# Kernel optimization log

Hardware: AMD Instinct MI355X
Metric: run time of the kernel (lower is better)

The kernel has to match this reference:

```python
import jax, jax.numpy as jnp
import numpy as np

SIGMAS = [1.0, 2.0, 4.0, 8.0, 16.0]
EPS = 0.05
ITERS = 30
N, M, D = 8192, 8192, 128


def _sqdist(X, Y):
    # ||x_i - y_j||^2, [n, m]
    d2 = (jnp.sum(X * X, axis=1)[:, None]
          + jnp.sum(Y * Y, axis=1)[None, :]
          - 2.0 * (X @ Y.T))
    return jnp.maximum(d2, 0.0)


def _ms_rbf(X, Y):
    d2 = _sqdist(X, Y)
    K = jnp.zeros_like(d2)
    for s in SIGMAS:  # small fixed loop over scales
        K = K + jnp.exp(-d2 / (2.0 * s * s))
    return K / float(len(SIGMAS))


def _sinkhorn_uniform(cost, eps, iters):
    n, m = cost.shape
    dtype = cost.dtype
    log_a = jnp.asarray(-np.log(float(n)), dtype)
    log_b = jnp.asarray(-np.log(float(m)), dtype)
    log_K = -(cost - jax.lax.stop_gradient(jnp.min(cost))) / eps

    def step(carry, _):
        log_u, log_v = carry
        log_u = log_a - jax.scipy.special.logsumexp(log_K + log_v[None, :], axis=1)
        log_v = log_b - jax.scipy.special.logsumexp(log_K + log_u[:, None], axis=0)
        return (log_u, log_v), None

    init = (jnp.zeros((n,), dtype), jnp.zeros((m,), dtype))
    (log_u, log_v), _ = jax.lax.scan(step, init, None, length=iters)
    return jnp.exp(log_u[:, None] + log_K + log_v[None, :])


def setup_inputs() -> dict:
    key = jax.random.key(0)
    kx, ky = jax.random.split(key)
    X = jax.random.normal(kx, (N, D), dtype=jnp.float32)
    Y = jax.random.normal(ky, (M, D), dtype=jnp.float32)
    return {"X": X, "Y": Y}


def reference(X, Y):
    Kxx = jnp.mean(_ms_rbf(X, X))
    Kyy = jnp.mean(_ms_rbf(Y, Y))
    Kxy = _ms_rbf(X, Y)
    cost = 1.0 / float(X.shape[0] * Y.shape[0]) - Kxy
    Gamma = _sinkhorn_uniform(cost, EPS, ITERS)
    Kxy_weighted = jnp.sum(Gamma * Kxy)
    return Kxx + Kyy - 2.0 * Kxy_weighted
```

## Files before the change

### kernel.cpp

```cpp
#include <hip/hip_runtime.h>
#include <math.h>

#define NR 8192
#define DDIM 128

static constexpr float LOG_AB2 = -13.0f;
static constexpr float OFF2    = -28.853900817779268f;
static constexpr float C8      = 0.11315255222658537f;
static constexpr float DQK8    = 1.0f / 255.0f;
static constexpr float E1 = -0.7213475204444817f;
static constexpr float E2 = -0.18033688011112043f;
static constexpr float E3 = -0.045084220027780107f;
static constexpr float E4 = -0.011271055006945027f;
static constexpr float E5 = -0.0028177637517362567f;

typedef __attribute__((ext_vector_type(8))) short  s16x8;
typedef __attribute__((ext_vector_type(4))) float  f32x4;

#if defined(__has_builtin)
#if __has_builtin(__builtin_amdgcn_exp2f)
#define EX2_IMPL(x) __builtin_amdgcn_exp2f(x)
#endif
#endif
#ifndef EX2_IMPL
extern "C" __device__ float __ocml_native_exp2_f32(float);
#define EX2_IMPL(x) __ocml_native_exp2_f32(x)
#endif
__device__ inline float ex2(float x) { return EX2_IMPL(x); }

__device__ inline unsigned short bf16rn(float f) {
    const unsigned u = __float_as_uint(f);
    return (unsigned short)((u + 0x7FFFu + ((u >> 16) & 1u)) >> 16);
}

__global__ __launch_bounds__(256) void conv_k(const float* __restrict__ X,
                                              unsigned short* __restrict__ hi,
                                              unsigned short* __restrict__ lo) {
    const int i = blockIdx.x * 1024 + threadIdx.x * 4;
    const float4 v = *reinterpret_cast<const float4*>(&X[i]);
    const float f[4] = {v.x, v.y, v.z, v.w};
    ushort4 h, l;
    unsigned short hh[4], ll[4];
#pragma unroll
    for (int j = 0; j < 4; ++j) {
        const unsigned short a = bf16rn(f[j]);
        const float hf = __uint_as_float((unsigned)a << 16);
        hh[j] = a;
        ll[j] = bf16rn(f[j] - hf);
    }
    h.x = hh[0]; h.y = hh[1]; h.z = hh[2]; h.w = hh[3];
    l.x = ll[0]; l.y = ll[1]; l.z = ll[2]; l.w = ll[3];
    *reinterpret_cast<ushort4*>(&hi[i]) = h;
    *reinterpret_cast<ushort4*>(&lo[i]) = l;
}

__global__ __launch_bounds__(256) void rownorm_k(const float* __restrict__ X,
                                                 float* __restrict__ nrm) {
    const int lane = threadIdx.x & 63;
    const int w    = threadIdx.x >> 6;
    const int row  = blockIdx.x * 4 + w;
    const float2 v = *reinterpret_cast<const float2*>(&X[(size_t)row * DDIM + lane * 2]);
    float s = v.x * v.x + v.y * v.y;
#pragma unroll
    for (int off = 32; off; off >>= 1) s += __shfl_xor(s, off);
    if (lane == 0) nrm[row] = s;
}

template <int MODE>
__global__ __launch_bounds__(256) void gemm_mfma_k(const unsigned short* __restrict__ XH,
                                                   const unsigned short* __restrict__ XL,
                                                   const unsigned short* __restrict__ YH,
                                                   const unsigned short* __restrict__ YL,
                                                   const float* __restrict__ nxp,
                                                   const float* __restrict__ nyp,
                                                   unsigned char* __restrict__ K8,
                                                   double* __restrict__ sums) {
    int bm, bn;
    const unsigned short *AH, *AL, *BH, *BL;
    const float *na, *nb;
    if (MODE == 0) {
        bm = blockIdx.x; bn = blockIdx.y;
        AH = XH; AL = XL; BH = YH; BL = YL; na = nxp; nb = nyp;
    } else {
        const int lin = blockIdx.x;
        int i = (int)((129.0f - sqrtf(16641.0f - 8.0f * (float)lin)) * 0.5f);
        while (i * 64 - i * (i - 1) / 2 > lin) --i;
        while ((i + 1) * 64 - (i + 1) * i / 2 <= lin) ++i;
        bm = i;
        bn = i + (lin - (i * 64 - i * (i - 1) / 2));
        const int sel = blockIdx.y;
        AH = BH = sel ? YH : XH;
        AL = BL = sel ? YL : XL;
        na = nb = sel ? nyp : nxp;
    }
    __shared__ unsigned short AsH[128 * 40], AsL[128 * 40], BsH[128 * 40], BsL[128 * 40];

    const int t    = threadIdx.x;
    const int lane = t & 63;
    const int w    = t >> 6;
    const int wr   = w >> 1, wc = w & 1;
    const int l15  = lane & 15, lg = lane >> 4;

    f32x4 acc[4][4];
#pragma unroll
    for (int mi = 0; mi < 4; ++mi)
#pragma unroll
        for (int ni = 0; ni < 4; ++ni) acc[mi][ni] = (f32x4){0.f, 0.f, 0.f, 0.f};

    const unsigned short* gAH = AH + (size_t)(bm * 128) * DDIM;
    const unsigned short* gAL = AL + (size_t)(bm * 128) * DDIM;
    const unsigned short* gBH = BH + (size_t)(bn * 128) * DDIM;
    const unsigned short* gBL = BL + (size_t)(bn * 128) * DDIM;

    for (int kc = 0; kc < 4; ++kc) {
        const int k0 = kc * 32;
        __syncthreads();
#pragma unroll
        for (int q = 0; q < 2; ++q) {
            const int idx = t + q * 256;
            const int row = idx >> 2, seg = idx & 3;
            const int go = row * DDIM + k0 + seg * 8;
            const int so = row * 40 + seg * 8;
            *reinterpret_cast<uint4*>(&AsH[so]) = *reinterpret_cast<const uint4*>(&gAH[go]);
            *reinterpret_cast<uint4*>(&AsL[so]) = *reinterpret_cast<const uint4*>(&gAL[go]);
            *reinterpret_cast<uint4*>(&BsH[so]) = *reinterpret_cast<const uint4*>(&gBH[go]);
            *reinterpret_cast<uint4*>(&BsL[so]) = *reinterpret_cast<const uint4*>(&gBL[go]);
        }
        __syncthreads();

        s16x8 bh[4], bl[4];
#pragma unroll
        for (int ni = 0; ni < 4; ++ni) {
            const int off = (wc * 64 + ni * 16 + l15) * 40 + lg * 8;
            bh[ni] = *reinterpret_cast<const s16x8*>(&BsH[off]);
            bl[ni] = *reinterpret_cast<const s16x8*>(&BsL[off]);
        }
#pragma unroll
        for (int mi = 0; mi < 4; ++mi) {
            const int off = (wr * 64 + mi * 16 + l15) * 40 + lg * 8;
            const s16x8 ah = *reinterpret_cast<const s16x8*>(&AsH[off]);
            const s16x8 al = *reinterpret_cast<const s16x8*>(&AsL[off]);
#pragma unroll
            for (int ni = 0; ni < 4; ++ni) {
                acc[mi][ni] = __builtin_amdgcn_mfma_f32_16x16x32_bf16(ah, bh[ni], acc[mi][ni], 0, 0, 0);
                acc[mi][ni] = __builtin_amdgcn_mfma_f32_16x16x32_bf16(ah, bl[ni], acc[mi][ni], 0, 0, 0);
                acc[mi][ni] = __builtin_amdgcn_mfma_f32_16x16x32_bf16(al, bh[ni], acc[mi][ni], 0, 0, 0);
            }
        }
    }

    const int mBase = bm * 128 + wr * 64;
    const int nBase = bn * 128 + wc * 64;
    float nbv[4];
#pragma unroll
    for (int ni = 0; ni < 4; ++ni) nbv[ni] = nb[nBase + ni * 16 + l15];

    if (MODE == 0) {
#pragma unroll
        for (int mi = 0; mi < 4; ++mi) {
#pragma unroll
            for (int j = 0; j < 4; ++j) {
                const int m = mBase + mi * 16 + lg * 4 + j;
                const float nav = na[m];
                unsigned char* krow = &K8[(size_t)m * NR + nBase + l15];
#pragma unroll
                for (int ni = 0; ni < 4; ++ni) {
                    float d2 = fmaf(-2.f, acc[mi][ni][j], nav + nbv[ni]);
                    d2 = fmaxf(d2, 0.f);
                    const float kv = 0.2f * (ex2(d2 * E1) + ex2(d2 * E2) + ex2(d2 * E3) +
                                             ex2(d2 * E4) + ex2(d2 * E5));
                    krow[ni * 16] = (unsigned char)__float2uint_rn(kv * 255.f);
                }
            }
        }
    } else {
        double lsum = 0.0;
#pragma unroll
        for (int mi = 0; mi < 4; ++mi) {
#pragma unroll
            for (int j = 0; j < 4; ++j) {
                const int m = mBase + mi * 16 + lg * 4 + j;
                const float nav = na[m];
                float rs = 0.f;
#pragma unroll
                for (int ni = 0; ni < 4; ++ni) {
                    float d2 = fmaf(-2.f, acc[mi][ni][j], nav + nbv[ni]);
                    d2 = fmaxf(d2, 0.f);
                    rs += 0.2f * (ex2(d2 * E1) + ex2(d2 * E2) + ex2(d2 * E3) +
                                  ex2(d2 * E4) + ex2(d2 * E5));
                }
                lsum += (double)rs;
            }
        }
        if (bn > bm) lsum *= 2.0;
#pragma unroll
        for (int o = 32; o; o >>= 1) lsum += __shfl_xor(lsum, o);
        if (lane == 0) atomicAdd(&sums[1 + blockIdx.y], lsum);
    }
}

__global__ __launch_bounds__(256) void init_lv_k(float* __restrict__ log_v) {
    log_v[blockIdx.x * 256 + threadIdx.x] = OFF2;
}

__global__ __launch_bounds__(256) void sink_row_k(const unsigned char* __restrict__ K8,
                                                  const float* __restrict__ log_v,
                                                  float* __restrict__ log_u) {
    __shared__ float red[4][8];
    const int t  = threadIdx.x;
    const int r0 = blockIdx.x * 8;
    const float4* Lv4 = reinterpret_cast<const float4*>(log_v);
    float s[8];
#pragma unroll
    for (int r = 0; r < 8; ++r) s[r] = 0.f;
#pragma unroll
    for (int p = 0; p < 2; ++p) {
        const int g = t + p * 256;
        const float4 l0 = Lv4[4 * g + 0];
        const float4 l1 = Lv4[4 * g + 1];
        const float4 l2 = Lv4[4 * g + 2];
        const float4 l3 = Lv4[4 * g + 3];
        const float lvv[16] = {l0.x, l0.y, l0.z, l0.w, l1.x, l1.y, l1.z, l1.w,
                               l2.x, l2.y, l2.z, l2.w, l3.x, l3.y, l3.z, l3.w};
        const uint4* col = reinterpret_cast<const uint4*>(K8 + (size_t)r0 * NR) + g;
#pragma unroll
        for (int r = 0; r < 8; ++r) {
            const uint4 w = col[(size_t)r * 512];
            const unsigned wd[4] = {w.x, w.y, w.z, w.w};
#pragma unroll
            for (int d = 0; d < 4; ++d) {
                const unsigned a = wd[d];
                s[r] += ex2(fmaf((float)(a & 255u),          C8, lvv[4 * d + 0]))
                      + ex2(fmaf((float)((a >> 8) & 255u),   C8, lvv[4 * d + 1]))
                      + ex2(fmaf((float)((a >> 16) & 255u),  C8, lvv[4 * d + 2]))
                      + ex2(fmaf((float)(a >> 24),           C8, lvv[4 * d + 3]));
            }
        }
    }
    const int lane = t & 63, w = t >> 6;
#pragma unroll
    for (int r = 0; r < 8; ++r) {
        float v = s[r];
#pragma unroll
        for (int o = 32; o; o >>= 1) v += __shfl_xor(v, o);
        if (lane == 0) red[w][r] = v;
    }
    __syncthreads();
    if (t < 8) {
        const float stot = (red[0][t] + red[1][t]) + (red[2][t] + red[3][t]);
        log_u[r0 + t] = LOG_AB2 - __log2f(stot) + OFF2;
    }
}

__global__ __launch_bounds__(256) void sink_colp_k(const unsigned char* __restrict__ K8,
                                                   const float* __restrict__ log_u,
                                                   float* __restrict__ ps) {
    const int t  = threadIdx.x;
    const int cg = blockIdx.x * 256 + t;
    const int rc = blockIdx.y;
    const uint4* base = reinterpret_cast<const uint4*>(K8) + (size_t)rc * 32 * 512 + cg;
    const float* lu = log_u + rc * 32;
    float s16[16];
#pragma unroll
    for (int e = 0; e < 16; ++e) s16[e] = 0.f;
#pragma unroll 4
    for (int r = 0; r < 32; ++r) {
        const uint4 w = base[(size_t)r * 512];
        const float lur = lu[r];
        const unsigned wd[4] = {w.x, w.y, w.z, w.w};
#pragma unroll
        for (int d = 0; d < 4; ++d) {
            const unsigned a = wd[d];
            s16[4 * d + 0] += ex2(fmaf((float)(a & 255u),         C8, lur));
            s16[4 * d + 1] += ex2(fmaf((float)((a >> 8) & 255u),  C8, lur));
            s16[4 * d + 2] += ex2(fmaf((float)((a >> 16) & 255u), C8, lur));
            s16[4 * d + 3] += ex2(fmaf((float)(a >> 24),          C8, lur));
        }
    }
    float4* pv = reinterpret_cast<float4*>(ps + (size_t)rc * NR + cg * 16);
#pragma unroll
    for (int d = 0; d < 4; ++d)
        pv[d] = {s16[4 * d + 0], s16[4 * d + 1], s16[4 * d + 2], s16[4 * d + 3]};
}

__global__ __launch_bounds__(256) void sink_combine_k(const float* __restrict__ ps,
                                                      float* __restrict__ log_v) {
    __shared__ float red[4][64];
    const int lane = threadIdx.x & 63;
    const int grp  = threadIdx.x >> 6;
    const int col  = blockIdx.x * 64 + lane;
    float s = 0.f;
#pragma unroll 8
    for (int c = grp * 64; c < grp * 64 + 64; ++c) s += ps[(size_t)c * NR + col];
    red[grp][lane] = s;
    __syncthreads();
    if (grp == 0) {
        const float stot = (red[0][lane] + red[1][lane]) + (red[2][lane] + red[3][lane]);
        log_v[col] = LOG_AB2 - __log2f(stot) + OFF2;
    }
}

__global__ __launch_bounds__(256) void gamma_sum_k(const unsigned char* __restrict__ K8,
                                                   const float* __restrict__ log_u,
                                                   const float* __restrict__ log_v,
                                                   double* __restrict__ S) {
    const int t  = threadIdx.x;
    const int cg = blockIdx.x * 256 + t;
    const int rc = blockIdx.y;
    float lvp[16];
#pragma unroll
    for (int e = 0; e < 16; ++e) lvp[e] = log_v[cg * 16 + e] - OFF2;
    const uint4* base = reinterpret_cast<const uint4*>(K8) + (size_t)rc * 32 * 512 + cg;
    const float* lu = log_u + rc * 32;
    double acc = 0.0;
#pragma unroll 4
    for (int r = 0; r < 32; ++r) {
        const uint4 w = base[(size_t)r * 512];
        const float lur = lu[r];
        const unsigned wd[4] = {w.x, w.y, w.z, w.w};
        float rs = 0.f;
#pragma unroll
        for (int d = 0; d < 4; ++d) {
            const unsigned a = wd[d];
            const float q0 = (float)(a & 255u);
            const float q1 = (float)((a >> 8) & 255u);
            const float q2 = (float)((a >> 16) & 255u);
            const float q3 = (float)(a >> 24);
            rs = fmaf(ex2(fmaf(q0, C8, lur + lvp[4 * d + 0])), q0, rs);
            rs = fmaf(ex2(fmaf(q1, C8, lur + lvp[4 * d + 1])), q1, rs);
            rs = fmaf(ex2(fmaf(q2, C8, lur + lvp[4 * d + 2])), q2, rs);
            rs = fmaf(ex2(fmaf(q3, C8, lur + lvp[4 * d + 3])), q3, rs);
        }
        acc += (double)rs;
    }
#pragma unroll
    for (int o = 32; o; o >>= 1) acc += __shfl_xor(acc, o);
    if ((t & 63) == 0) atomicAdd(S, acc);
}

__global__ void finalize_k(const double* __restrict__ scal, float* __restrict__ out) {
    const double inv = 1.0 / (8192.0 * 8192.0);
    out[0] = (float)(scal[1] * inv + scal[2] * inv - 2.0 * (double)DQK8 * scal[3]);
}

extern "C" void kernel_launch(void* const* d_in, const int* in_sizes, int n_in,
                              void* d_out, int out_size, void* d_ws, size_t ws_size,
                              hipStream_t stream) {
    const float* X = (const float*)d_in[0];
    const float* Y = (const float*)d_in[1];

    char* ws = (char*)d_ws;
    unsigned char* K8 = (unsigned char*)ws;
    float* nx    = (float*)(ws + 67108864);
    float* ny    = nx + NR;
    float* log_u = ny + NR;
    float* log_v = log_u + NR;
    char*  scal  = (char*)(log_v + NR);
    double* scal_d = (double*)scal;
    float* ps = (float*)(scal + 512);
    unsigned short* XH = (unsigned short*)(ws + 75629056);
    unsigned short* XL = XH + NR * DDIM;
    unsigned short* YH = XL + NR * DDIM;
    unsigned short* YL = YH + NR * DDIM;
    const size_t needed = 75629056 + 4 * (size_t)NR * DDIM * 2;
    if (ws_size < needed) return;

    hipMemsetAsync(scal, 0, 512, stream);

    conv_k<<<NR * DDIM / 1024, 256, 0, stream>>>(X, XH, XL);
    conv_k<<<NR * DDIM / 1024, 256, 0, stream>>>(Y, YH, YL);
    rownorm_k<<<NR / 4, 256, 0, stream>>>(X, nx);
    rownorm_k<<<NR / 4, 256, 0, stream>>>(Y, ny);

    gemm_mfma_k<0><<<dim3(64, 64), 256, 0, stream>>>(XH, XL, YH, YL, nx, ny, K8, scal_d);
    gemm_mfma_k<1><<<dim3(2080, 2), 256, 0, stream>>>(XH, XL, YH, YL, nx, ny, nullptr, scal_d);

    init_lv_k<<<NR / 256, 256, 0, stream>>>(log_v);

    for (int it = 0; it < 30; ++it) {
        sink_row_k<<<NR / 8, 256, 0, stream>>>(K8, log_v, log_u);
        sink_colp_k<<<dim3(2, 256), 256, 0, stream>>>(K8, log_u, ps);
        sink_combine_k<<<128, 256, 0, stream>>>(ps, log_v);
    }

    gamma_sum_k<<<dim3(2, 256), 256, 0, stream>>>(K8, log_u, log_v, scal_d + 3);
    finalize_k<<<1, 1, 0, stream>>>(scal_d, (float*)d_out);
}
```

Measured before the change: 1.603 ms.

## Replace split-bf16 GEMM with single fp16 MFMA and direct global-to-LDS loads

Drops the hi/lo bf16 split (three MFMAs per tile) in favour of a single fp16 conversion with one MFMA per tile. Operand tiles are now staged with global_load_lds into one swizzled shared buffer, so the register round-trip and the padded layout are no longer needed. This cuts MFMA work and conversion/memory traffic for the distance GEMMs. In exchange, the dot products lose precision (fp16 has an 11-bit mantissa), which may shift the quantized kernel values and the Sinkhorn result.

```diff
diff --git a/kernel.cpp b/kernel.cpp
--- a/kernel.cpp
+++ b/kernel.cpp
@@ -14,8 +14,8 @@
 static constexpr float E4 = -0.011271055006945027f;
 static constexpr float E5 = -0.0028177637517362567f;
 
-typedef __attribute__((ext_vector_type(8))) short  s16x8;
-typedef __attribute__((ext_vector_type(4))) float  f32x4;
+typedef __attribute__((ext_vector_type(8))) _Float16 f16x8;
+typedef __attribute__((ext_vector_type(4))) float    f32x4;
 
 #if defined(__has_builtin)
 #if __has_builtin(__builtin_amdgcn_exp2f)
@@ -28,30 +28,26 @@
 #endif
 __device__ inline float ex2(float x) { return EX2_IMPL(x); }
 
-__device__ inline unsigned short bf16rn(float f) {
-    const unsigned u = __float_as_uint(f);
-    return (unsigned short)((u + 0x7FFFu + ((u >> 16) & 1u)) >> 16);
-}
-
-__global__ __launch_bounds__(256) void conv_k(const float* __restrict__ X,
-                                              unsigned short* __restrict__ hi,
-                                              unsigned short* __restrict__ lo) {
+typedef const unsigned int __attribute__((address_space(1)))* gas_ptr;
+typedef unsigned int __attribute__((address_space(3)))*       las_ptr;
+__device__ inline void gload16(const void* g, void* l) {
+    __builtin_amdgcn_global_load_lds((gas_ptr)g, (las_ptr)l, 16, 0, 0);
+}
+
+__device__ inline unsigned short f2h(float f) {
+    return __builtin_bit_cast(unsigned short, (_Float16)f);
+}
+
+__global__ __launch_bounds__(256) void convh_k(const float* __restrict__ X,
+                                               unsigned short* __restrict__ H) {
     const int i = blockIdx.x * 1024 + threadIdx.x * 4;
     const float4 v = *reinterpret_cast<const float4*>(&X[i]);
-    const float f[4] = {v.x, v.y, v.z, v.w};
-    ushort4 h, l;
-    unsigned short hh[4], ll[4];
-#pragma unroll
-    for (int j = 0; j < 4; ++j) {
-        const unsigned short a = bf16rn(f[j]);
-        const float hf = __uint_as_float((unsigned)a << 16);
-        hh[j] = a;
-        ll[j] = bf16rn(f[j] - hf);
-    }
-    h.x = hh[0]; h.y = hh[1]; h.z = hh[2]; h.w = hh[3];
-    l.x = ll[0]; l.y = ll[1]; l.z = ll[2]; l.w = ll[3];
-    *reinterpret_cast<ushort4*>(&hi[i]) = h;
-    *reinterpret_cast<ushort4*>(&lo[i]) = l;
+    ushort4 h;
+    h.x = f2h(v.x);
+    h.y = f2h(v.y);
+    h.z = f2h(v.z);
+    h.w = f2h(v.w);
+    *reinterpret_cast<ushort4*>(&H[i]) = h;
 }
 
 __global__ __launch_bounds__(256) void rownorm_k(const float* __restrict__ X,
@@ -67,20 +63,18 @@
 }
 
 template <int MODE>
-__global__ __launch_bounds__(256) void gemm_mfma_k(const unsigned short* __restrict__ XH,
-                                                   const unsigned short* __restrict__ XL,
-                                                   const unsigned short* __restrict__ YH,
-                                                   const unsigned short* __restrict__ YL,
+__global__ __launch_bounds__(256) void gemm_mfma_k(const unsigned short* __restrict__ XF,
+                                                   const unsigned short* __restrict__ YF,
                                                    const float* __restrict__ nxp,
                                                    const float* __restrict__ nyp,
                                                    unsigned char* __restrict__ K8,
                                                    double* __restrict__ sums) {
     int bm, bn;
-    const unsigned short *AH, *AL, *BH, *BL;
+    const unsigned short *A, *B;
     const float *na, *nb;
     if (MODE == 0) {
         bm = blockIdx.x; bn = blockIdx.y;
-        AH = XH; AL = XL; BH = YH; BL = YL; na = nxp; nb = nyp;
+        A = XF; B = YF; na = nxp; nb = nyp;
     } else {
         const int lin = blockIdx.x;
         int i = (int)((129.0f - sqrtf(16641.0f - 8.0f * (float)lin)) * 0.5f);
@@ -89,11 +83,10 @@
         bm = i;
         bn = i + (lin - (i * 64 - i * (i - 1) / 2));
         const int sel = blockIdx.y;
-        AH = BH = sel ? YH : XH;
-        AL = BL = sel ? YL : XL;
+        A = B = sel ? YF : XF;
         na = nb = sel ? nyp : nxp;
     }
-    __shared__ unsigned short AsH[128 * 40], AsL[128 * 40], BsH[128 * 40], BsL[128 * 40];
+    __shared__ unsigned short Tile[128 * 64];
 
     const int t    = threadIdx.x;
     const int lane = t & 63;
@@ -101,51 +94,43 @@
     const int wr   = w >> 1, wc = w & 1;
     const int l15  = lane & 15, lg = lane >> 4;
 
+    const int lr = lane >> 3;
+    const int u  = (lane & 7) ^ lr;
+    const int ss = u & 3;
+
     f32x4 acc[4][4];
 #pragma unroll
     for (int mi = 0; mi < 4; ++mi)
 #pragma unroll
         for (int ni = 0; ni < 4; ++ni) acc[mi][ni] = (f32x4){0.f, 0.f, 0.f, 0.f};
 
-    const unsigned short* gAH = AH + (size_t)(bm * 128) * DDIM;
-    const unsigned short* gAL = AL + (size_t)(bm * 128) * DDIM;
-    const unsigned short* gBH = BH + (size_t)(bn * 128) * DDIM;
-    const unsigned short* gBL = BL + (size_t)(bn * 128) * DDIM;
+    const unsigned short* src = (u < 4)
+        ? A + (size_t)(bm * 128 + lr) * DDIM + ss * 8
+        : B + (size_t)(bn * 128 + lr) * DDIM + ss * 8;
 
     for (int kc = 0; kc < 4; ++kc) {
-        const int k0 = kc * 32;
+        if (kc) __syncthreads();
+        const int ko = kc * 32;
+#pragma unroll
+        for (int c = 0; c < 4; ++c) {
+            const int row0 = w * 32 + c * 8;
+            gload16(src + (size_t)row0 * DDIM + ko, &Tile[row0 * 64]);
+        }
         __syncthreads();
-#pragma unroll
-        for (int q = 0; q < 2; ++q) {
-            const int idx = t + q * 256;
-            const int row = idx >> 2, seg = idx & 3;
-            const int go = row * DDIM + k0 + seg * 8;
-            const int so = row * 40 + seg * 8;
-            *reinterpret_cast<uint4*>(&AsH[so]) = *reinterpret_cast<const uint4*>(&gAH[go]);
-            *reinterpret_cast<uint4*>(&AsL[so]) = *reinterpret_cast<const uint4*>(&gAL[go]);
-            *reinterpret_cast<uint4*>(&BsH[so]) = *reinterpret_cast<const uint4*>(&gBH[go]);
-            *reinterpret_cast<uint4*>(&BsL[so]) = *reinterpret_cast<const uint4*>(&gBL[go]);
-        }
-        __syncthreads();
-
-        s16x8 bh[4], bl[4];
+
+        f16x8 bf[4];
 #pragma unroll
         for (int ni = 0; ni < 4; ++ni) {
-            const int off = (wc * 64 + ni * 16 + l15) * 40 + lg * 8;
-            bh[ni] = *reinterpret_cast<const s16x8*>(&BsH[off]);
-            bl[ni] = *reinterpret_cast<const s16x8*>(&BsL[off]);
+            const int R = wc * 64 + ni * 16 + l15;
+            bf[ni] = *reinterpret_cast<const f16x8*>(&Tile[R * 64 + ((4 + lg) ^ (R & 7)) * 8]);
         }
 #pragma unroll
         for (int mi = 0; mi < 4; ++mi) {
-            const int off = (wr * 64 + mi * 16 + l15) * 40 + lg * 8;
-            const s16x8 ah = *reinterpret_cast<const s16x8*>(&AsH[off]);
-            const s16x8 al = *reinterpret_cast<const s16x8*>(&AsL[off]);
-#pragma unroll
-            for (int ni = 0; ni < 4; ++ni) {
-                acc[mi][ni] = __builtin_amdgcn_mfma_f32_16x16x32_bf16(ah, bh[ni], acc[mi][ni], 0, 0, 0);
-                acc[mi][ni] = __builtin_amdgcn_mfma_f32_16x16x32_bf16(ah, bl[ni], acc[mi][ni], 0, 0, 0);
-                acc[mi][ni] = __builtin_amdgcn_mfma_f32_16x16x32_bf16(al, bh[ni], acc[mi][ni], 0, 0, 0);
-            }
+            const int R = wr * 64 + mi * 16 + l15;
+            const f16x8 af = *reinterpret_cast<const f16x8*>(&Tile[R * 64 + (lg ^ (R & 7)) * 8]);
+#pragma unroll
+            for (int ni = 0; ni < 4; ++ni)
+                acc[mi][ni] = __builtin_amdgcn_mfma_f32_16x16x32_f16(af, bf[ni], acc[mi][ni], 0, 0, 0);
         }
     }
 
@@ -225,8 +210,8 @@
         const uint4* col = reinterpret_cast<const uint4*>(K8 + (size_t)r0 * NR) + g;
 #pragma unroll
         for (int r = 0; r < 8; ++r) {
-            const uint4 w = col[(size_t)r * 512];
-            const unsigned wd[4] = {w.x, w.y, w.z, w.w};
+            const uint4 wq = col[(size_t)r * 512];
+            const unsigned wd[4] = {wq.x, wq.y, wq.z, wq.w};
 #pragma unroll
             for (int d = 0; d < 4; ++d) {
                 const unsigned a = wd[d];
@@ -237,13 +222,13 @@
             }
         }
     }
-    const int lane = t & 63, w = t >> 6;
+    const int lane = t & 63, wv = t >> 6;
 #pragma unroll
     for (int r = 0; r < 8; ++r) {
         float v = s[r];
 #pragma unroll
         for (int o = 32; o; o >>= 1) v += __shfl_xor(v, o);
-        if (lane == 0) red[w][r] = v;
+        if (lane == 0) red[wv][r] = v;
     }
     __syncthreads();
     if (t < 8) {
@@ -255,19 +240,19 @@
 __global__ __launch_bounds__(256) void sink_colp_k(const unsigned char* __restrict__ K8,
                                                    const float* __restrict__ log_u,
                                                    float* __restrict__ ps) {
-    const int t  = threadIdx.x;
-    const int cg = blockIdx.x * 256 + t;
-    const int rc = blockIdx.y;
-    const uint4* base = reinterpret_cast<const uint4*>(K8) + (size_t)rc * 32 * 512 + cg;
+    const int t   = threadIdx.x;
+    const int cg4 = blockIdx.x * 256 + t;
+    const int rc  = blockIdx.y;
+    const uint4* base = reinterpret_cast<const uint4*>(K8) + (size_t)rc * 32 * 512 + cg4;
     const float* lu = log_u + rc * 32;
     float s16[16];
 #pragma unroll
     for (int e = 0; e < 16; ++e) s16[e] = 0.f;
 #pragma unroll 4
     for (int r = 0; r < 32; ++r) {
-        const uint4 w = base[(size_t)r * 512];
+        const uint4 wq = base[(size_t)r * 512];
         const float lur = lu[r];
-        const unsigned wd[4] = {w.x, w.y, w.z, w.w};
+        const unsigned wd[4] = {wq.x, wq.y, wq.z, wq.w};
 #pragma unroll
         for (int d = 0; d < 4; ++d) {
             const unsigned a = wd[d];
@@ -277,7 +262,7 @@
             s16[4 * d + 3] += ex2(fmaf((float)(a >> 24),          C8, lur));
         }
     }
-    float4* pv = reinterpret_cast<float4*>(ps + (size_t)rc * NR + cg * 16);
+    float4* pv = reinterpret_cast<float4*>(ps + (size_t)rc * NR + cg4 * 16);
 #pragma unroll
     for (int d = 0; d < 4; ++d)
         pv[d] = {s16[4 * d + 0], s16[4 * d + 1], s16[4 * d + 2], s16[4 * d + 3]};
@@ -304,13 +289,13 @@
                                                    const float* __restrict__ log_u,
                                                    const float* __restrict__ log_v,
                                                    double* __restrict__ S) {
-    const int t  = threadIdx.x;
-    const int cg = blockIdx.x * 256 + t;
-    const int rc = blockIdx.y;
+    const int t   = threadIdx.x;
+    const int cg4 = blockIdx.x * 256 + t;
+    const int rc  = blockIdx.y;
     float lvp[16];
 #pragma unroll
-    for (int e = 0; e < 16; ++e) lvp[e] = log_v[cg * 16 + e] - OFF2;
-    const uint4* base = reinterpret_cast<const uint4*>(K8) + (size_t)rc * 32 * 512 + cg;
+    for (int e = 0; e < 16; ++e) lvp[e] = log_v[cg4 * 16 + e] - OFF2;
+    const uint4* base = reinterpret_cast<const uint4*>(K8) + (size_t)rc * 32 * 512 + cg4;
     const float* lu = log_u + rc * 32;
     double acc = 0.0;
 #pragma unroll 4
@@ -358,22 +343,20 @@
     char*  scal  = (char*)(log_v + NR);
     double* scal_d = (double*)scal;
     float* ps = (float*)(scal + 512);
-    unsigned short* XH = (unsigned short*)(ws + 75629056);
-    unsigned short* XL = XH + NR * DDIM;
-    unsigned short* YH = XL + NR * DDIM;
-    unsigned short* YL = YH + NR * DDIM;
-    const size_t needed = 75629056 + 4 * (size_t)NR * DDIM * 2;
+    unsigned short* XF = (unsigned short*)(ws + 75629056);
+    unsigned short* YF = XF + NR * DDIM;
+    const size_t needed = 75629056 + 2 * (size_t)NR * DDIM * 2;
     if (ws_size < needed) return;
 
-    hipMemsetAsync(scal, 0, 512, stream);
-
-    conv_k<<<NR * DDIM / 1024, 256, 0, stream>>>(X, XH, XL);
-    conv_k<<<NR * DDIM / 1024, 256, 0, stream>>>(Y, YH, YL);
+    (void)hipMemsetAsync(scal, 0, 512, stream);
+
+    convh_k<<<NR * DDIM / 1024, 256, 0, stream>>>(X, XF);
+    convh_k<<<NR * DDIM / 1024, 256, 0, stream>>>(Y, YF);
     rownorm_k<<<NR / 4, 256, 0, stream>>>(X, nx);
     rownorm_k<<<NR / 4, 256, 0, stream>>>(Y, ny);
 
-    gemm_mfma_k<0><<<dim3(64, 64), 256, 0, stream>>>(XH, XL, YH, YL, nx, ny, K8, scal_d);
-    gemm_mfma_k<1><<<dim3(2080, 2), 256, 0, stream>>>(XH, XL, YH, YL, nx, ny, nullptr, scal_d);
+    gemm_mfma_k<0><<<dim3(64, 64), 256, 0, stream>>>(XF, YF, nx, ny, K8, scal_d);
+    gemm_mfma_k<1><<<dim3(2080, 2), 256, 0, stream>>>(XF, YF, nx, ny, nullptr, scal_d);
 
     init_lv_k<<<NR / 256, 256, 0, stream>>>(log_v);
 
```

After: 1.572 ms. 2.0% less time.
